# Kernel tuning notes

Measured on AMD Instinct MI355X. Metric: run time of the kernel, lower is better.

The kernel has to match this reference:

```python
import jax, jax.numpy as jnp
import numpy as np

N, E, IN, D, G, C = 100000, 3200000, 128, 512, 64, 10
EPS = 1e-5

def _bn(x, g, b):
    # training-mode BatchNorm1d: batch statistics, biased variance
    m = jnp.mean(x, axis=0)
    v = jnp.var(x, axis=0)
    return (x - m) * jax.lax.rsqrt(v + EPS) * g + b

def _prelu(x, a):
    return jnp.where(x >= 0, x, a * x)

def setup_inputs() -> dict:
    key = jax.random.key(0)
    ks = jax.random.split(key, 16)
    def w(k, shape):
        fan_in = shape[0]
        s = 1.0 / np.sqrt(fan_in)
        return jax.random.uniform(k, shape, jnp.float32, -s, s)
    inp = {
        'x': jax.random.normal(ks[0], (N, IN), jnp.float32),
        'edge_index': jax.random.randint(ks[1], (2, E), 0, N),
        'batch': jnp.sort(jax.random.randint(ks[2], (N,), 0, G)),
        'bn1_g': jnp.ones((IN,), jnp.float32), 'bn1_b': jnp.zeros((IN,), jnp.float32),
        'w0': w(ks[3], (IN, D)), 'b0': jnp.zeros((D,), jnp.float32),
        'w1': w(ks[4], (D, D)), 'bb1': jnp.zeros((D,), jnp.float32),
        'w2': w(ks[5], (D, D)), 'bb2': jnp.zeros((D,), jnp.float32),
        'w3': w(ks[6], (D, D)), 'bb3': jnp.zeros((D,), jnp.float32),
        'bn3_g': jnp.ones((D,), jnp.float32), 'bn3_b': jnp.zeros((D,), jnp.float32),
        'a3': jnp.array([0.25], jnp.float32),
        'fc1_w': w(ks[7], (D, D)), 'fc1_b': jnp.zeros((D,), jnp.float32),
        'fc2_w': w(ks[8], (D, D // 2)), 'fc2_b': jnp.zeros((D // 2,), jnp.float32),
        'fc3_w': w(ks[9], (D // 2, C)), 'fc3_b': jnp.zeros((C,), jnp.float32),
    }
    return inp

def reference(x, edge_index, batch, bn1_g, bn1_b, w0, b0, w1, bb1, w2, bb2, w3, bb3,
              bn3_g, bn3_b, a3, fc1_w, fc1_b, fc2_w, fc2_b, fc3_w, fc3_b):
    # ChebConv with K=1 reduces to a plain linear layer (T_0(L)x = x); edge_index unused.
    h = _bn(x, bn1_g, bn1_b)
    h = jax.nn.relu(h @ w0 + b0)
    for w_, b_ in ((w1, bb1), (w2, bb2), (w3, bb3)):
        h = jax.nn.relu(h @ w_ + b_)
        h = _bn(h, bn3_g, bn3_b)   # same bn3 module reused each layer
    # global_add_pool: segment-sum of node features per graph
    h = jax.ops.segment_sum(h, batch, num_segments=G)
    h = _prelu(h @ fc1_w + fc1_b, a3)
    h = jax.nn.sigmoid(h @ fc2_w + fc2_b)
    return h @ fc3_w + fc3_b
```

## Files before the change

kernel.cpp:

```cpp
#include <hip/hip_runtime.h>
#include <math.h>

#define NN 100000
#define INF 128
#define DD  512
#define GG  64
#define CC  10

typedef __bf16 bf16;
typedef __bf16 bf16x8 __attribute__((ext_vector_type(8)));
typedef __bf16 bf16x4 __attribute__((ext_vector_type(4)));
typedef float  f32x4  __attribute__((ext_vector_type(4)));
typedef unsigned int u32x4 __attribute__((ext_vector_type(4)));

__device__ __forceinline__ void gld16(const bf16* g, bf16* l) {
    __builtin_amdgcn_global_load_lds(
        (const __attribute__((address_space(1))) unsigned int*)g,
        (__attribute__((address_space(3))) unsigned int*)l, 16, 0, 0);
}


__global__ void zero_k(float* __restrict__ p, int n) {
    int i = blockIdx.x * blockDim.x + threadIdx.x;
    if (i < n) p[i] = 0.0f;
}

__global__ void bounds_k(const int* __restrict__ batch, int* __restrict__ starts) {
    int g = threadIdx.x;
    if (g <= GG) {
        int lo = 0, hi = NN;
        while (lo < hi) {
            int mid = (lo + hi) >> 1;
            if (batch[mid] < g) lo = mid + 1; else hi = mid;
        }
        starts[g] = lo;
    }
}

__global__ __launch_bounds__(256)
void colstats_cvt(const float* __restrict__ x, bf16* __restrict__ xb,
                  float* __restrict__ stats) {
    __shared__ float rs[4][128], rq[4][128];
    int t = threadIdx.x;
    int w = t >> 6, l = t & 63;
    int rg = t >> 5;
    int cq = t & 31;
    float s0 = 0, s1 = 0, s2 = 0, s3 = 0, q0 = 0, q1 = 0, q2 = 0, q3 = 0;
    for (int row = blockIdx.x * 8 + rg; row < NN; row += gridDim.x * 8) {
        float4 v = *(const float4*)&x[(size_t)row * INF + cq * 4];
        bf16x4 o; o[0] = (bf16)v.x; o[1] = (bf16)v.y; o[2] = (bf16)v.z; o[3] = (bf16)v.w;
        *(bf16x4*)&xb[(size_t)row * INF + cq * 4] = o;
        s0 += v.x; q0 += v.x * v.x;
        s1 += v.y; q1 += v.y * v.y;
        s2 += v.z; q2 += v.z * v.z;
        s3 += v.w; q3 += v.w * v.w;
    }
    s0 += __shfl_xor(s0, 32); s1 += __shfl_xor(s1, 32);
    s2 += __shfl_xor(s2, 32); s3 += __shfl_xor(s3, 32);
    q0 += __shfl_xor(q0, 32); q1 += __shfl_xor(q1, 32);
    q2 += __shfl_xor(q2, 32); q3 += __shfl_xor(q3, 32);
    if (l < 32) {
        rs[w][cq * 4 + 0] = s0; rs[w][cq * 4 + 1] = s1;
        rs[w][cq * 4 + 2] = s2; rs[w][cq * 4 + 3] = s3;
        rq[w][cq * 4 + 0] = q0; rq[w][cq * 4 + 1] = q1;
        rq[w][cq * 4 + 2] = q2; rq[w][cq * 4 + 3] = q3;
    }
    __syncthreads();
    if (t < 128) {
        atomicAdd(&stats[t],       rs[0][t] + rs[1][t] + rs[2][t] + rs[3][t]);
        atomicAdd(&stats[INF + t], rq[0][t] + rq[1][t] + rq[2][t] + rq[3][t]);
    }
}

__global__ void prep_st(const float* __restrict__ stats, int K,
                        const float* __restrict__ gamma, const float* __restrict__ beta,
                        float* __restrict__ s, float* __restrict__ t) {
    int j = blockIdx.x * blockDim.x + threadIdx.x;
    if (j < K) {
        const float invN = 1.0f / (float)NN;
        float mean = stats[j] * invN;
        float var  = stats[K + j] * invN - mean * mean;
        float sv   = gamma[j] * rsqrtf(var + 1e-5f);
        s[j] = sv;
        t[j] = beta[j] - mean * sv;
    }
}

__global__ __launch_bounds__(256)
void fold_wt(const float* __restrict__ s, const float* __restrict__ W,
             bf16* __restrict__ Wt, int K) {
    __shared__ float tile[64][68];
    __shared__ float sarr[64];
    int j0 = blockIdx.x * 64, k0 = blockIdx.y * 64;
    int t = threadIdx.x;
    if (t < 64) sarr[t] = s ? s[k0 + t] : 1.0f;
    int kk = t >> 2, jq = t & 3;
#pragma unroll
    for (int i = 0; i < 4; i++) {
        float4 v = *(const float4*)&W[(size_t)(k0 + kk) * DD + j0 + jq * 16 + i * 4];
        *(float4*)&tile[kk][jq * 16 + i * 4] = v;
    }
    __syncthreads();
    int jj = t >> 2, kq = t & 3;
    bf16 ov[16];
#pragma unroll
    for (int i = 0; i < 16; i++)
        ov[i] = (bf16)(tile[kq * 16 + i][jj] * sarr[kq * 16 + i]);
    bf16* dst = &Wt[(size_t)(j0 + jj) * K + k0 + kq * 16];
    *(u32x4*)dst       = *(u32x4*)&ov[0];
    *(u32x4*)(dst + 8) = *(u32x4*)&ov[8];
}

__global__ __launch_bounds__(256)
void fold_b(const float* __restrict__ tv, const float* __restrict__ W,
            const float* __restrict__ b, float* __restrict__ bp, int K) {
    __shared__ float red[4][64];
    int jj = threadIdx.x & 63, kr = threadIdx.x >> 6;
    int j = blockIdx.x * 64 + jj;
    float acc = 0.f;
    for (int k = kr; k < K; k += 4)
        acc += tv[k] * W[(size_t)k * DD + j];
    red[kr][jj] = acc;
    __syncthreads();
    if (kr == 0) bp[j] = b[j] + red[0][jj] + red[1][jj] + red[2][jj] + red[3][jj];
}

template <int K, int MODE>
__global__ __launch_bounds__(256, 4)
void gemm_mfma(const bf16* __restrict__ A, const bf16* __restrict__ Wt,
               const float* __restrict__ bias, bf16* __restrict__ H, int M,
               float* __restrict__ stats, const int* __restrict__ batch,
               float* __restrict__ R) {
    __shared__ bf16 smem[18432];
    bf16* As = smem;
    bf16* Bs = smem + 8192;
    const int t  = threadIdx.x;
    const int l  = t & 63;
    const int w  = t >> 6;
    const int wr = w >> 1, wc = w & 1;
    const int col0 = blockIdx.x * 128;
    const int row0 = blockIdx.y * 128;

    const int srow = w * 8 + (l >> 3);
    const int sslt = l & 7;

    f32x4 acc[4][4];
#pragma unroll
    for (int m = 0; m < 4; m++)
#pragma unroll
        for (int n = 0; n < 4; n++) acc[m][n] = (f32x4){0.f, 0.f, 0.f, 0.f};

#pragma unroll 1
    for (int k0 = 0; k0 < K; k0 += 64) {
#pragma unroll
        for (int c = 0; c < 4; c++) {
            int r  = c * 32 + srow;
            int sg = sslt ^ (r & 7);
            int ga = row0 + r; if (ga >= M) ga = M - 1;
            gld16(A  + (size_t)ga * K + k0 + sg * 8,
                  (bf16*)((char*)As + c * 4096 + w * 1024));
            gld16(Wt + (size_t)(col0 + r) * K + k0 + sg * 8,
                  (bf16*)((char*)Bs + c * 4096 + w * 1024));
        }
        __syncthreads();
#pragma unroll
        for (int ks = 0; ks < 2; ks++) {
            bf16x8 af[4], bfr[4];
#pragma unroll
            for (int m = 0; m < 4; m++) {
                int r = wr * 64 + m * 16 + (l & 15);
                af[m] = *(const bf16x8*)((const char*)As + r * 128 +
                        ((((ks << 2) + (l >> 4)) ^ (r & 7)) << 4));
            }
#pragma unroll
            for (int n = 0; n < 4; n++) {
                int r = wc * 64 + n * 16 + (l & 15);
                bfr[n] = *(const bf16x8*)((const char*)Bs + r * 128 +
                         ((((ks << 2) + (l >> 4)) ^ (r & 7)) << 4));
            }
#pragma unroll
            for (int m = 0; m < 4; m++)
#pragma unroll
                for (int n = 0; n < 4; n++)
                    acc[m][n] = __builtin_amdgcn_mfma_f32_16x16x32_bf16(af[m], bfr[n], acc[m][n], 0, 0, 0);
        }
        __syncthreads();
    }

    float csumA[4], csqA[4];

    if (MODE <= 1) {
        bf16* ct = smem;
#pragma unroll
        for (int n = 0; n < 4; n++) {
            int lc = wc * 64 + n * 16 + (l & 15);
            float bv = bias[col0 + lc];
            float cs = 0.f, cq = 0.f;
#pragma unroll
            for (int m = 0; m < 4; m++) {
#pragma unroll
                for (int q = 0; q < 4; q++) {
                    int lr = wr * 64 + m * 16 + (l >> 4) * 4 + q;
                    float v = acc[m][n][q] + bv;
                    v = v > 0.f ? v : 0.f;
                    ct[lr * 136 + lc] = (bf16)v;
                    if (MODE == 1 && row0 + lr < M) { cs += v; cq += v * v; }
                }
            }
            csumA[n] = cs; csqA[n] = cq;
        }
        __syncthreads();
        {
            const char* cts = (const char*)ct;
            char* Hc = (char*)H;
#pragma unroll
            for (int i = 0; i < 8; i++) {
                int fo = i * 4096 + t * 16;
                int r  = fo >> 8;
                int cb = fo & 255;
                if (row0 + r < M)
                    *(u32x4*)(Hc + ((size_t)(row0 + r) * (DD * 2) + (size_t)col0 * 2 + cb)) =
                        *(const u32x4*)(cts + r * 272 + cb);
            }
        }
    } else {
        int gid[4][4];
#pragma unroll
        for (int m = 0; m < 4; m++)
#pragma unroll
            for (int q = 0; q < 4; q++) {
                int grow = row0 + wr * 64 + m * 16 + (l >> 4) * 4 + q;
                gid[m][q] = (grow < M) ? batch[grow] : -1;
            }
#pragma unroll
        for (int n = 0; n < 4; n++) {
            int col = col0 + wc * 64 + n * 16 + (l & 15);
            float bv = bias[col];
            float cs = 0.f, cq = 0.f;
            float ps = 0.f; int gc = -1;
#pragma unroll
            for (int m = 0; m < 4; m++) {
#pragma unroll
                for (int q = 0; q < 4; q++) {
                    int g = gid[m][q];
                    if (g >= 0) {
                        float v = acc[m][n][q] + bv;
                        v = v > 0.f ? v : 0.f;
                        cs += v; cq += v * v;
                        if (g != gc) {
                            if (gc >= 0) atomicAdd(&R[(size_t)gc * DD + col], ps);
                            ps = 0.f; gc = g;
                        }
                        ps += v;
                    }
                }
            }
            if (gc >= 0) atomicAdd(&R[(size_t)gc * DD + col], ps);
            csumA[n] = cs; csqA[n] = cq;
        }
    }

    if (MODE >= 1) {
#pragma unroll
        for (int n = 0; n < 4; n++) {
            float cs = csumA[n], cq = csqA[n];
            cs += __shfl_xor(cs, 16); cs += __shfl_xor(cs, 32);
            cq += __shfl_xor(cq, 16); cq += __shfl_xor(cq, 32);
            if ((l >> 4) == 0) {
                int col = col0 + wc * 64 + n * 16 + l;
                atomicAdd(&stats[col], cs);
                atomicAdd(&stats[DD + col], cq);
            }
        }
    }
}

__global__ __launch_bounds__(512)
void pool_fin(const float* __restrict__ R, const int* __restrict__ starts,
              const float* __restrict__ s4, const float* __restrict__ t4,
              float* __restrict__ P) {
    int g = blockIdx.x, j = threadIdx.x;
    float cnt = (float)(starts[g + 1] - starts[g]);
    P[g * DD + j] = R[(size_t)g * DD + j] * s4[j] + cnt * t4[j];
}

__global__ __launch_bounds__(256)
void head_k(const float* __restrict__ P,
            const float* __restrict__ fc1_w, const float* __restrict__ fc1_b,
            const float* __restrict__ fc2_w, const float* __restrict__ fc2_b,
            const float* __restrict__ fc3_w, const float* __restrict__ fc3_b,
            const float* __restrict__ a3, float* __restrict__ out) {
    __shared__ float p[DD], y1[DD], y2[DD / 2];
    int g = blockIdx.x, t = threadIdx.x;
    p[t]       = P[g * DD + t];
    p[t + 256] = P[g * DD + t + 256];
    __syncthreads();
    float alpha = a3[0];

    float acc0 = fc1_b[t], acc1 = fc1_b[t + 256];
    for (int k = 0; k < DD; k++) {
        float pv = p[k];
        acc0 = fmaf(pv, fc1_w[(size_t)k * DD + t], acc0);
        acc1 = fmaf(pv, fc1_w[(size_t)k * DD + t + 256], acc1);
    }
    y1[t]       = acc0 >= 0.f ? acc0 : alpha * acc0;
    y1[t + 256] = acc1 >= 0.f ? acc1 : alpha * acc1;
    __syncthreads();

    float acc = fc2_b[t];
    for (int k = 0; k < DD; k++) acc = fmaf(y1[k], fc2_w[(size_t)k * (DD / 2) + t], acc);
    y2[t] = 1.0f / (1.0f + expf(-acc));
    __syncthreads();

    if (t < CC) {
        float a = fc3_b[t];
        for (int k = 0; k < DD / 2; k++) a = fmaf(y2[k], fc3_w[(size_t)k * CC + t], a);
        out[g * CC + t] = a;
    }
}

extern "C" void kernel_launch(void* const* d_in, const int* in_sizes, int n_in,
                              void* d_out, int out_size, void* d_ws, size_t ws_size,
                              hipStream_t stream) {
    const float* x     = (const float*)d_in[0];
    const int*   batch = (const int*)d_in[2];
    const float* bn1_g = (const float*)d_in[3];
    const float* bn1_b = (const float*)d_in[4];
    const float* w0    = (const float*)d_in[5];
    const float* b0    = (const float*)d_in[6];
    const float* w1    = (const float*)d_in[7];
    const float* bb1   = (const float*)d_in[8];
    const float* w2    = (const float*)d_in[9];
    const float* bb2   = (const float*)d_in[10];
    const float* w3    = (const float*)d_in[11];
    const float* bb3   = (const float*)d_in[12];
    const float* bn3_g = (const float*)d_in[13];
    const float* bn3_b = (const float*)d_in[14];
    const float* a3    = (const float*)d_in[15];
    const float* fc1_w = (const float*)d_in[16];
    const float* fc1_b = (const float*)d_in[17];
    const float* fc2_w = (const float*)d_in[18];
    const float* fc2_b = (const float*)d_in[19];
    const float* fc3_w = (const float*)d_in[20];
    const float* fc3_b = (const float*)d_in[21];
    float* out = (float*)d_out;

    char* base = (char*)d_ws;
    const size_t HBYTES = (size_t)NN * DD * 2;
    bf16* Ha = (bf16*)base;
    bf16* Hb = (bf16*)(base + HBYTES);
    bf16* Xb = Hb;
    bf16* Wt = (bf16*)(base + 2 * HBYTES);
    float* f = (float*)(base + 2 * HBYTES + 524288);
    size_t off = 0;
    float* stats  = f + off; off += 3328;
    float* R      = f + off; off += (size_t)GG * DD;
    float* statsX = stats;
    float* stats2 = stats + 256;
    float* stats3 = stats + 1280;
    float* stats4 = stats + 2304;
    float* s1 = f + off; off += 128;
    float* t1 = f + off; off += 128;
    float* s2 = f + off; off += 512;
    float* t2 = f + off; off += 512;
    float* s3 = f + off; off += 512;
    float* t3 = f + off; off += 512;
    float* s4 = f + off; off += 512;
    float* t4 = f + off; off += 512;
    float* b0p = f + off; off += 512;
    float* bp  = f + off; off += 512;
    float* P   = f + off; off += (size_t)GG * DD;
    int*   starts = (int*)(f + off); off += 128;

    (void)in_sizes; (void)n_in; (void)out_size; (void)ws_size;

    const dim3 ggrid(4, (NN + 127) / 128);
    const int kZeroCount = 3328 + GG * DD;

    zero_k<<<(kZeroCount + 255) / 256, 256, 0, stream>>>(stats, kZeroCount);
    bounds_k<<<1, 128, 0, stream>>>(batch, starts);

    colstats_cvt<<<256, 256, 0, stream>>>(x, Xb, statsX);
    prep_st<<<1, 128, 0, stream>>>(statsX, 128, bn1_g, bn1_b, s1, t1);
    fold_wt<<<dim3(8, INF / 64), 256, 0, stream>>>(s1, w0, Wt, INF);
    fold_b<<<8, 256, 0, stream>>>(t1, w0, b0, b0p, INF);
    gemm_mfma<INF, 0><<<ggrid, 256, 0, stream>>>(Xb, Wt, b0p, Ha, NN, nullptr, nullptr, nullptr);

    fold_wt<<<dim3(8, DD / 64), 256, 0, stream>>>(nullptr, w1, Wt, DD);
    gemm_mfma<DD, 1><<<ggrid, 256, 0, stream>>>(Ha, Wt, bb1, Hb, NN, stats2, nullptr, nullptr);

    prep_st<<<2, 256, 0, stream>>>(stats2, 512, bn3_g, bn3_b, s2, t2);
    fold_wt<<<dim3(8, DD / 64), 256, 0, stream>>>(s2, w2, Wt, DD);
    fold_b<<<8, 256, 0, stream>>>(t2, w2, bb2, bp, DD);
    gemm_mfma<DD, 1><<<ggrid, 256, 0, stream>>>(Hb, Wt, bp, Ha, NN, stats3, nullptr, nullptr);

    prep_st<<<2, 256, 0, stream>>>(stats3, 512, bn3_g, bn3_b, s3, t3);
    fold_wt<<<dim3(8, DD / 64), 256, 0, stream>>>(s3, w3, Wt, DD);
    fold_b<<<8, 256, 0, stream>>>(t3, w3, bb3, bp, DD);
    gemm_mfma<DD, 2><<<ggrid, 256, 0, stream>>>(Ha, Wt, bp, nullptr, NN, stats4, batch, R);

    prep_st<<<2, 256, 0, stream>>>(stats4, 512, bn3_g, bn3_b, s4, t4);
    pool_fin<<<GG, 512, 0, stream>>>(R, starts, s4, t4, P);
    head_k<<<GG, 256, 0, stream>>>(P, fc1_w, fc1_b, fc2_w, fc2_b, fc3_w, fc3_b, a3, out);
}
```

Measured before the change: 605.5 us.

## Remap GEMM blocks per XCD for L2 reuse and fold BN prep into consumers

GEMM launches become 1-D and are remapped so each XCD processes a contiguous range of row blocks, with all four column tiles of a row block scheduled on the same XCD, aiming to reuse A tiles in that XCD's L2. The separate prep_st kernels are removed; BN scale/shift are recomputed inline inside fold_wt, fold_b and pool_fin, cutting four launches. The cost is redundant per-block recomputation of the BN scale and shift, plus a few excess GEMM blocks that exit early.

New measurement: 603.6 us. Within noise of the previous version (-0.3%).

```diff
diff --git a/kernel.cpp b/kernel.cpp
--- a/kernel.cpp
+++ b/kernel.cpp
@@ -13,10 +13,30 @@
 typedef float  f32x4  __attribute__((ext_vector_type(4)));
 typedef unsigned int u32x4 __attribute__((ext_vector_type(4)));
 
+#define NRB ((NN + 127) / 128)
+#define CPX ((NRB + 7) / 8)
+#define GEMM_GRID (8 * CPX * 4)
+
 __device__ __forceinline__ void gld16(const bf16* g, bf16* l) {
     __builtin_amdgcn_global_load_lds(
         (const __attribute__((address_space(1))) unsigned int*)g,
         (__attribute__((address_space(3))) unsigned int*)l, 16, 0, 0);
+}
+
+__device__ __forceinline__ float bn_s(const float* stats, const float* gamma,
+                                      int K, int k) {
+    const float invN = 1.0f / (float)NN;
+    float mean = stats[k] * invN;
+    float var  = stats[K + k] * invN - mean * mean;
+    return gamma[k] * rsqrtf(var + 1e-5f);
+}
+__device__ __forceinline__ float bn_t(const float* stats, const float* gamma,
+                                      const float* beta, int K, int k) {
+    const float invN = 1.0f / (float)NN;
+    float mean = stats[k] * invN;
+    float var  = stats[K + k] * invN - mean * mean;
+    float sv   = gamma[k] * rsqrtf(var + 1e-5f);
+    return beta[k] - mean * sv;
 }
 
 
@@ -72,28 +92,14 @@
     }
 }
 
-__global__ void prep_st(const float* __restrict__ stats, int K,
-                        const float* __restrict__ gamma, const float* __restrict__ beta,
-                        float* __restrict__ s, float* __restrict__ t) {
-    int j = blockIdx.x * blockDim.x + threadIdx.x;
-    if (j < K) {
-        const float invN = 1.0f / (float)NN;
-        float mean = stats[j] * invN;
-        float var  = stats[K + j] * invN - mean * mean;
-        float sv   = gamma[j] * rsqrtf(var + 1e-5f);
-        s[j] = sv;
-        t[j] = beta[j] - mean * sv;
-    }
-}
-
 __global__ __launch_bounds__(256)
-void fold_wt(const float* __restrict__ s, const float* __restrict__ W,
-             bf16* __restrict__ Wt, int K) {
+void fold_wt(const float* __restrict__ stats, const float* __restrict__ gamma,
+             const float* __restrict__ W, bf16* __restrict__ Wt, int K) {
     __shared__ float tile[64][68];
     __shared__ float sarr[64];
     int j0 = blockIdx.x * 64, k0 = blockIdx.y * 64;
     int t = threadIdx.x;
-    if (t < 64) sarr[t] = s ? s[k0 + t] : 1.0f;
+    if (t < 64) sarr[t] = stats ? bn_s(stats, gamma, K, k0 + t) : 1.0f;
     int kk = t >> 2, jq = t & 3;
 #pragma unroll
     for (int i = 0; i < 4; i++) {
@@ -112,14 +118,19 @@
 }
 
 __global__ __launch_bounds__(256)
-void fold_b(const float* __restrict__ tv, const float* __restrict__ W,
+void fold_b(const float* __restrict__ stats, const float* __restrict__ gamma,
+            const float* __restrict__ beta, const float* __restrict__ W,
             const float* __restrict__ b, float* __restrict__ bp, int K) {
     __shared__ float red[4][64];
-    int jj = threadIdx.x & 63, kr = threadIdx.x >> 6;
+    __shared__ float tt[DD];
+    int t = threadIdx.x;
+    for (int k = t; k < K; k += 256) tt[k] = bn_t(stats, gamma, beta, K, k);
+    __syncthreads();
+    int jj = t & 63, kr = t >> 6;
     int j = blockIdx.x * 64 + jj;
     float acc = 0.f;
     for (int k = kr; k < K; k += 4)
-        acc += tv[k] * W[(size_t)k * DD + j];
+        acc += tt[k] * W[(size_t)k * DD + j];
     red[kr][jj] = acc;
     __syncthreads();
     if (kr == 0) bp[j] = b[j] + red[0][jj] + red[1][jj] + red[2][jj] + red[3][jj];
@@ -131,6 +142,14 @@
                const float* __restrict__ bias, bf16* __restrict__ H, int M,
                float* __restrict__ stats, const int* __restrict__ batch,
                float* __restrict__ R) {
+    const int id  = blockIdx.x;
+    const int xcd = id & 7;
+    const int jj  = id >> 3;
+    const int yb  = xcd * CPX + (jj >> 2);
+    if (yb >= NRB) return;
+    const int col0 = (jj & 3) * 128;
+    const int row0 = yb * 128;
+
     __shared__ bf16 smem[18432];
     bf16* As = smem;
     bf16* Bs = smem + 8192;
@@ -138,8 +157,6 @@
     const int l  = t & 63;
     const int w  = t >> 6;
     const int wr = w >> 1, wc = w & 1;
-    const int col0 = blockIdx.x * 128;
-    const int row0 = blockIdx.y * 128;
 
     const int srow = w * 8 + (l >> 3);
     const int sslt = l & 7;
@@ -277,11 +294,13 @@
 
 __global__ __launch_bounds__(512)
 void pool_fin(const float* __restrict__ R, const int* __restrict__ starts,
-              const float* __restrict__ s4, const float* __restrict__ t4,
-              float* __restrict__ P) {
+              const float* __restrict__ stats, const float* __restrict__ gamma,
+              const float* __restrict__ beta, float* __restrict__ P) {
     int g = blockIdx.x, j = threadIdx.x;
+    float sv = bn_s(stats, gamma, DD, j);
+    float tv = bn_t(stats, gamma, beta, DD, j);
     float cnt = (float)(starts[g + 1] - starts[g]);
-    P[g * DD + j] = R[(size_t)g * DD + j] * s4[j] + cnt * t4[j];
+    P[g * DD + j] = R[(size_t)g * DD + j] * sv + cnt * tv;
 }
 
 __global__ __launch_bounds__(256)
@@ -359,14 +378,6 @@
     float* stats2 = stats + 256;
     float* stats3 = stats + 1280;
     float* stats4 = stats + 2304;
-    float* s1 = f + off; off += 128;
-    float* t1 = f + off; off += 128;
-    float* s2 = f + off; off += 512;
-    float* t2 = f + off; off += 512;
-    float* s3 = f + off; off += 512;
-    float* t3 = f + off; off += 512;
-    float* s4 = f + off; off += 512;
-    float* t4 = f + off; off += 512;
     float* b0p = f + off; off += 512;
     float* bp  = f + off; off += 512;
     float* P   = f + off; off += (size_t)GG * DD;
@@ -374,32 +385,27 @@
 
     (void)in_sizes; (void)n_in; (void)out_size; (void)ws_size;
 
-    const dim3 ggrid(4, (NN + 127) / 128);
     const int kZeroCount = 3328 + GG * DD;
 
     zero_k<<<(kZeroCount + 255) / 256, 256, 0, stream>>>(stats, kZeroCount);
     bounds_k<<<1, 128, 0, stream>>>(batch, starts);
 
     colstats_cvt<<<256, 256, 0, stream>>>(x, Xb, statsX);
-    prep_st<<<1, 128, 0, stream>>>(statsX, 128, bn1_g, bn1_b, s1, t1);
-    fold_wt<<<dim3(8, INF / 64), 256, 0, stream>>>(s1, w0, Wt, INF);
-    fold_b<<<8, 256, 0, stream>>>(t1, w0, b0, b0p, INF);
-    gemm_mfma<INF, 0><<<ggrid, 256, 0, stream>>>(Xb, Wt, b0p, Ha, NN, nullptr, nullptr, nullptr);
-
-    fold_wt<<<dim3(8, DD / 64), 256, 0, stream>>>(nullptr, w1, Wt, DD);
-    gemm_mfma<DD, 1><<<ggrid, 256, 0, stream>>>(Ha, Wt, bb1, Hb, NN, stats2, nullptr, nullptr);
-
-    prep_st<<<2, 256, 0, stream>>>(stats2, 512, bn3_g, bn3_b, s2, t2);
-    fold_wt<<<dim3(8, DD / 64), 256, 0, stream>>>(s2, w2, Wt, DD);
-    fold_b<<<8, 256, 0, stream>>>(t2, w2, bb2, bp, DD);
-    gemm_mfma<DD, 1><<<ggrid, 256, 0, stream>>>(Hb, Wt, bp, Ha, NN, stats3, nullptr, nullptr);
-
-    prep_st<<<2, 256, 0, stream>>>(stats3, 512, bn3_g, bn3_b, s3, t3);
-    fold_wt<<<dim3(8, DD / 64), 256, 0, stream>>>(s3, w3, Wt, DD);
-    fold_b<<<8, 256, 0, stream>>>(t3, w3, bb3, bp, DD);
-    gemm_mfma<DD, 2><<<ggrid, 256, 0, stream>>>(Ha, Wt, bp, nullptr, NN, stats4, batch, R);
-
-    prep_st<<<2, 256, 0, stream>>>(stats4, 512, bn3_g, bn3_b, s4, t4);
-    pool_fin<<<GG, 512, 0, stream>>>(R, starts, s4, t4, P);
+    fold_wt<<<dim3(8, INF / 64), 256, 0, stream>>>(statsX, bn1_g, w0, Wt, INF);
+    fold_b<<<8, 256, 0, stream>>>(statsX, bn1_g, bn1_b, w0, b0, b0p, INF);
+    gemm_mfma<INF, 0><<<GEMM_GRID, 256, 0, stream>>>(Xb, Wt, b0p, Ha, NN, nullptr, nullptr, nullptr);
+
+    fold_wt<<<dim3(8, DD / 64), 256, 0, stream>>>(nullptr, nullptr, w1, Wt, DD);
+    gemm_mfma<DD, 1><<<GEMM_GRID, 256, 0, stream>>>(Ha, Wt, bb1, Hb, NN, stats2, nullptr, nullptr);
+
+    fold_wt<<<dim3(8, DD / 64), 256, 0, stream>>>(stats2, bn3_g, w2, Wt, DD);
+    fold_b<<<8, 256, 0, stream>>>(stats2, bn3_g, bn3_b, w2, bb2, bp, DD);
+    gemm_mfma<DD, 1><<<GEMM_GRID, 256, 0, stream>>>(Hb, Wt, bp, Ha, NN, stats3, nullptr, nullptr);
+
+    fold_wt<<<dim3(8, DD / 64), 256, 0, stream>>>(stats3, bn3_g, w3, Wt, DD);
+    fold_b<<<8, 256, 0, stream>>>(stats3, bn3_g, bn3_b, w3, bb3, bp, DD);
+    gemm_mfma<DD, 2><<<GEMM_GRID, 256, 0, stream>>>(Ha, Wt, bp, nullptr, NN, stats4, batch, R);
+
+    pool_fin<<<GG, 512, 0, stream>>>(R, starts, stats4, bn3_g, bn3_b, P);
     head_k<<<GG, 256, 0, stream>>>(P, fc1_w, fc1_b, fc2_w, fc2_b, fc3_w, fc3_b, a3, out);
 }
```
